# Optimization experiments

Measured on AMD Instinct MI355X. Metric: run time of the kernel, lower is better.

The kernel has to match this reference:

```python
import jax, jax.numpy as jnp
import numpy as np

N_NODES = 50000
N_EDGES = 800000
N_REL = 4
F_IN = 128
H1 = 64          # RGCN out
HEADS = 4
D_H = 32         # per-head GAT out
N_GRAPHS = 64


def setup_inputs() -> dict:
    key = jax.random.key(0)
    ks = jax.random.split(key, 16)
    inp = {
        "x": jax.random.normal(ks[0], (N_NODES, F_IN), dtype=jnp.float32),
        "edge_index": jax.random.randint(ks[1], (2, N_EDGES), 0, N_NODES, dtype=jnp.int32),
        "edge_type": jax.random.randint(ks[2], (N_EDGES,), 0, N_REL, dtype=jnp.int32),
        "batch": jnp.sort(jax.random.randint(ks[3], (N_NODES,), 0, N_GRAPHS, dtype=jnp.int32)),
        # RGCNConv params (relation weights, root weight, bias)
        "W_rel": jax.random.normal(ks[4], (N_REL, F_IN, H1), dtype=jnp.float32) * 0.05,
        "W_root": jax.random.normal(ks[5], (F_IN, H1), dtype=jnp.float32) * 0.05,
        "b_rgcn": jnp.zeros((H1,), dtype=jnp.float32),
        # GATConv params
        "W_gat": jax.random.normal(ks[6], (H1, HEADS * D_H), dtype=jnp.float32) * 0.1,
        "att_src": jax.random.normal(ks[7], (HEADS, D_H), dtype=jnp.float32) * 0.1,
        "att_dst": jax.random.normal(ks[8], (HEADS, D_H), dtype=jnp.float32) * 0.1,
        "b_gat": jnp.zeros((HEADS * D_H,), dtype=jnp.float32),
        # dense layers
        "W1": jax.random.normal(ks[9], (HEADS * D_H, 16), dtype=jnp.float32) * 0.05,
        "b1": jnp.zeros((16,), dtype=jnp.float32),
        "W2": jax.random.normal(ks[10], (16, 1), dtype=jnp.float32) * 0.2,
        "b2": jnp.zeros((1,), dtype=jnp.float32),
    }
    return inp


def reference(x, W_rel, W_root, b_rgcn, W_gat, att_src, att_dst, b_gat,
              W1, b1, W2, b2, edge_index, edge_type, batch):
    src, dst = edge_index[0], edge_index[1]
    n = x.shape[0]

    # ---- RGCNConv: mean aggregation per relation, then linear (linearity lets
    # us aggregate raw features first, then apply W_rel) + root transform ----
    xs = x[src]                                            # [E, F_IN]
    out = x @ W_root + b_rgcn                              # [N, H1]
    for r in range(N_REL):
        mask = (edge_type == r).astype(x.dtype)            # [E]
        s = jax.ops.segment_sum(xs * mask[:, None], dst, num_segments=n)
        cnt = jax.ops.segment_sum(mask, dst, num_segments=n)
        mean_r = s / jnp.maximum(cnt, 1.0)[:, None]        # [N, F_IN]
        out = out + mean_r @ W_rel[r]
    h = jax.nn.relu(out)                                   # [N, H1]
    # (dropout omitted: deterministic/eval reference)

    # ---- GATConv (heads=4, concat, no self loops, edge_attr unused) ----
    g = (h @ W_gat).reshape(n, HEADS, D_H)                 # [N, H, D]
    a_s = jnp.einsum('nhd,hd->nh', g, att_src)             # [N, H]
    a_d = jnp.einsum('nhd,hd->nh', g, att_dst)
    e = jax.nn.leaky_relu(a_s[src] + a_d[dst], 0.2)        # [E, H]
    m = jax.ops.segment_max(e, dst, num_segments=n)        # [N, H]
    ex = jnp.exp(e - m[dst])                               # [E, H]
    den = jax.ops.segment_sum(ex, dst, num_segments=n)     # [N, H]
    alpha = ex / den[dst]
    o = jax.ops.segment_sum(alpha[:, :, None] * g[src], dst, num_segments=n)
    o = o.reshape(n, HEADS * D_H) + b_gat                  # [N, 128]
    o = jax.nn.leaky_relu(o, 0.01)

    # ---- dense1 -> leaky_relu -> global max pool -> dense2 ----
    z = jax.nn.leaky_relu(o @ W1 + b1, 0.01)               # [N, 16]
    p = jax.ops.segment_max(z, batch, num_segments=N_GRAPHS)  # [G, 16]
    y = p @ W2 + b2                                        # [G, 1]
    return y
```

## Files before the change

kernel.cpp:

```cpp
#include <hip/hip_runtime.h>
#include <hip/hip_bf16.h>

constexpr int N_NODES = 50000;
constexpr int N_EDGES = 800000;
constexpr int F_IN = 128;
constexpr int H1 = 64;
constexpr int HEADS = 4;
constexpr int D_H = 32;
constexpr int HOUT = HEADS * D_H;
constexpr int N_REL = 4;
constexpr int N_GRAPHS = 64;
constexpr int MBIG = H1 * (1 + N_REL);
constexpr int NBLK = (N_NODES + 255) / 256;
constexpr int N_PAD = 50048;

typedef __attribute__((ext_vector_type(8))) short bf16x8;
typedef __attribute__((ext_vector_type(4))) float f32x4;

__device__ __forceinline__ unsigned f2mono(float f) {
  unsigned u = __float_as_uint(f);
  return (u & 0x80000000u) ? ~u : (u | 0x80000000u);
}
__device__ __forceinline__ float mono2f(unsigned m) {
  unsigned u = (m & 0x80000000u) ? (m & 0x7FFFFFFFu) : ~m;
  return __uint_as_float(u);
}
constexpr unsigned MONO_NEG_INF = 0x007FFFFFu;

__device__ __forceinline__ unsigned short f2bf(float f) {
  unsigned u = __float_as_uint(f);
  unsigned r = (u + 0x7FFFu + ((u >> 16) & 1u)) >> 16;
  return (unsigned short)r;
}
__device__ __forceinline__ float bf2f(unsigned short h) {
  return __uint_as_float((unsigned)h << 16);
}
__device__ __forceinline__ float bflo(unsigned u) { return __uint_as_float(u << 16); }
__device__ __forceinline__ float bfhi(unsigned u) { return __uint_as_float(u & 0xFFFF0000u); }

constexpr int XCVT_BLOCKS = (N_NODES * (F_IN / 4) + 255) / 256;
constexpr int HIST_BLOCKS = (N_EDGES + 255) / 256;
constexpr int WT_BLOCKS = (MBIG * F_IN + HOUT * H1 + 255) / 256;

__global__ __launch_bounds__(256) void pre_fused(
    const float* __restrict__ x,
    const float* __restrict__ W_root, const float* __restrict__ W_rel,
    const float* __restrict__ W_gat,
    const int* __restrict__ dst,
    unsigned short* __restrict__ xhi, unsigned short* __restrict__ xlo,
    unsigned short* __restrict__ WbT_hi, unsigned short* __restrict__ WbT_lo,
    unsigned short* __restrict__ WgT_hi, unsigned short* __restrict__ WgT_lo,
    int* __restrict__ deg, int* __restrict__ rank,
    unsigned* __restrict__ pm) {
  int b = blockIdx.x;
  if (b < XCVT_BLOCKS) {
    int i = b * 256 + threadIdx.x;
    if (i < N_NODES * (F_IN / 4)) {
      float4 v = reinterpret_cast<const float4*>(x)[i];
      ushort4 hi, lo;
      hi.x = f2bf(v.x); lo.x = f2bf(v.x - bf2f(hi.x));
      hi.y = f2bf(v.y); lo.y = f2bf(v.y - bf2f(hi.y));
      hi.z = f2bf(v.z); lo.z = f2bf(v.z - bf2f(hi.z));
      hi.w = f2bf(v.w); lo.w = f2bf(v.w - bf2f(hi.w));
      reinterpret_cast<ushort4*>(xhi)[i] = hi;
      reinterpret_cast<ushort4*>(xlo)[i] = lo;
    }
  } else if (b < XCVT_BLOCKS + HIST_BLOCKS) {
    int e = (b - XCVT_BLOCKS) * 256 + threadIdx.x;
    if (e < N_EDGES) rank[e] = atomicAdd(&deg[dst[e]], 1);
  } else if (b < XCVT_BLOCKS + HIST_BLOCKS + WT_BLOCKS) {
    int i = (b - XCVT_BLOCKS - HIST_BLOCKS) * 256 + threadIdx.x;
    if (i < MBIG * F_IN) {
      int c = i / F_IN, k = i % F_IN;
      float w = (c < H1) ? W_root[k * H1 + c]
                         : W_rel[((size_t)(((c - H1) >> 6) * F_IN + k)) * H1 + ((c - H1) & 63)];
      unsigned short hi = f2bf(w);
      WbT_hi[i] = hi;
      WbT_lo[i] = f2bf(w - bf2f(hi));
    } else {
      int j = i - MBIG * F_IN;
      if (j < HOUT * H1) {
        int c = j / H1, k = j % H1;
        float w = W_gat[k * HOUT + c];
        unsigned short hi = f2bf(w);
        WgT_hi[j] = hi;
        WgT_lo[j] = f2bf(w - bf2f(hi));
      }
    }
  } else {
    for (int i = threadIdx.x; i < N_GRAPHS * 16; i += 256) pm[i] = MONO_NEG_INF;
  }
}

template <int K>
__device__ __forceinline__ void gemm_body(int bx, int by,
    const unsigned short* __restrict__ Ahi_,
    const unsigned short* __restrict__ Alo_,
    const unsigned short* __restrict__ BT_hi,
    const unsigned short* __restrict__ BT_lo,
    unsigned short* __restrict__ Cbf, int N, int M) {
  __shared__ unsigned short Ah[64 * K];
  __shared__ unsigned short Al[64 * K];
  const int tid = threadIdx.x;
  const int rowBase = bx * 64;
  const int colBase = by * 64;
  constexpr int KQ8 = K / 8;
  for (int s = tid; s < 64 * KQ8; s += 256) {
    int r = s / KQ8, c8 = (s % KQ8) * 8;
    size_t gi = (size_t)(rowBase + r) * K + c8;
    int sw = c8 ^ ((r & 7) << 3);
    *reinterpret_cast<uint4*>(&Ah[r * K + sw]) =
        *reinterpret_cast<const uint4*>(&Ahi_[gi]);
    *reinterpret_cast<uint4*>(&Al[r * K + sw]) =
        *reinterpret_cast<const uint4*>(&Alo_[gi]);
  }
  __syncthreads();
  const int wv = tid >> 6, lane = tid & 63;
  const int wr = (wv >> 1) * 32, wc = (wv & 1) * 32;
  const int lrow = lane & 15, lkc = lane >> 4;
  f32x4 acc[2][2] = {};
#pragma unroll
  for (int ks = 0; ks < K; ks += 32) {
    bf16x8 ah[2], al[2], bh[2], bl[2];
#pragma unroll
    for (int fr = 0; fr < 2; ++fr) {
      int r = wr + fr * 16 + lrow;
      int sw = (ks + lkc * 8) ^ ((r & 7) << 3);
      ah[fr] = *reinterpret_cast<const bf16x8*>(&Ah[r * K + sw]);
      al[fr] = *reinterpret_cast<const bf16x8*>(&Al[r * K + sw]);
    }
#pragma unroll
    for (int fc = 0; fc < 2; ++fc) {
      int c = colBase + wc + fc * 16 + lrow;
      bh[fc] = *reinterpret_cast<const bf16x8*>(&BT_hi[(size_t)c * K + ks + lkc * 8]);
      bl[fc] = *reinterpret_cast<const bf16x8*>(&BT_lo[(size_t)c * K + ks + lkc * 8]);
    }
#pragma unroll
    for (int fr = 0; fr < 2; ++fr)
#pragma unroll
      for (int fc = 0; fc < 2; ++fc) {
        acc[fr][fc] = __builtin_amdgcn_mfma_f32_16x16x32_bf16(ah[fr], bh[fc], acc[fr][fc], 0, 0, 0);
        acc[fr][fc] = __builtin_amdgcn_mfma_f32_16x16x32_bf16(ah[fr], bl[fc], acc[fr][fc], 0, 0, 0);
        acc[fr][fc] = __builtin_amdgcn_mfma_f32_16x16x32_bf16(al[fr], bh[fc], acc[fr][fc], 0, 0, 0);
      }
  }
#pragma unroll
  for (int fr = 0; fr < 2; ++fr) {
#pragma unroll
    for (int i = 0; i < 4; ++i) {
      int row = rowBase + wr + fr * 16 + lkc * 4 + i;
      if (row < N) {
#pragma unroll
        for (int fc = 0; fc < 2; ++fc) {
          int col = colBase + wc + fc * 16 + lrow;
          Cbf[(size_t)row * M + col] = f2bf(acc[fr][fc][i]);
        }
      }
    }
  }
}

constexpr int G1_BX = N_PAD / 64;
constexpr int G1_BLOCKS = G1_BX * (MBIG / 64);
__global__ __launch_bounds__(256) void gemm1_fill(
    const unsigned short* __restrict__ xhi, const unsigned short* __restrict__ xlo,
    const unsigned short* __restrict__ wbt_hi, const unsigned short* __restrict__ wbt_lo,
    unsigned short* __restrict__ xtbf,
    const int* __restrict__ src, const int* __restrict__ dst,
    const int* __restrict__ etype, const int* __restrict__ off,
    const int* __restrict__ rank, int* __restrict__ eprep) {
  if (blockIdx.x < G1_BLOCKS) {
    gemm_body<128>(blockIdx.x % G1_BX, blockIdx.x / G1_BX,
                   xhi, xlo, wbt_hi, wbt_lo, xtbf, N_NODES, MBIG);
  } else {
    int e = (blockIdx.x - G1_BLOCKS) * 256 + threadIdx.x;
    if (e < N_EDGES) {
      int pos = off[dst[e]] + rank[e];
      eprep[pos] = src[e] | (etype[e] << 16);
    }
  }
}

__global__ __launch_bounds__(256) void gemm2_k(
    const unsigned short* __restrict__ hhi, const unsigned short* __restrict__ hlo,
    const unsigned short* __restrict__ wgt_hi, const unsigned short* __restrict__ wgt_lo,
    unsigned short* __restrict__ gbf) {
  gemm_body<64>(blockIdx.x % G1_BX, blockIdx.x / G1_BX,
                hhi, hlo, wgt_hi, wgt_lo, gbf, N_NODES, HOUT);
}

__global__ __launch_bounds__(256) void k_s1(const int* __restrict__ deg,
                                            int* __restrict__ bsum) {
  __shared__ int ss[256];
  int t = threadIdx.x;
  int i = blockIdx.x * 256 + t;
  ss[t] = (i < N_NODES) ? deg[i] : 0;
  __syncthreads();
  for (int d = 128; d > 0; d >>= 1) {
    if (t < d) ss[t] += ss[t + d];
    __syncthreads();
  }
  if (t == 0) bsum[blockIdx.x] = ss[0];
}

__global__ __launch_bounds__(256) void k_s2(const int* __restrict__ bsum,
                                            int* __restrict__ bbase,
                                            int* __restrict__ off) {
  __shared__ int ss[256];
  int t = threadIdx.x;
  int v = (t < NBLK) ? bsum[t] : 0;
  ss[t] = v;
  __syncthreads();
  for (int d = 1; d < 256; d <<= 1) {
    int u = (t >= d) ? ss[t - d] : 0;
    __syncthreads();
    ss[t] += u;
    __syncthreads();
  }
  if (t < NBLK) bbase[t] = ss[t] - v;
  if (t == NBLK - 1) off[N_NODES] = ss[t];
}

__global__ __launch_bounds__(256) void k_s3(const int* __restrict__ deg,
                                            const int* __restrict__ bbase,
                                            int* __restrict__ off) {
  __shared__ int ss[256];
  int t = threadIdx.x;
  int i = blockIdx.x * 256 + t;
  int v = (i < N_NODES) ? deg[i] : 0;
  ss[t] = v;
  __syncthreads();
  for (int d = 1; d < 256; d <<= 1) {
    int u = (t >= d) ? ss[t - d] : 0;
    __syncthreads();
    ss[t] += u;
    __syncthreads();
  }
  if (i < N_NODES) off[i] = bbase[blockIdx.x] + ss[t] - v;
}

__global__ __launch_bounds__(256) void rgcn_gather(const unsigned short* __restrict__ xtbf,
                                                   const int* __restrict__ off,
                                                   const int* __restrict__ eprep,
                                                   const float* __restrict__ b_rgcn,
                                                   unsigned short* __restrict__ hhi,
                                                   unsigned short* __restrict__ hlo) {
  int wid = (blockIdx.x * 256 + threadIdx.x) >> 6;
  int lane = threadIdx.x & 63;
  int half = lane >> 5;
  int cp = lane & 31;
  int start = off[wid], end = off[wid + 1];
  float a0x=0.f,a0y=0.f,a1x=0.f,a1y=0.f,a2x=0.f,a2y=0.f,a3x=0.f,a3y=0.f;
  int c0=0,c1=0,c2=0,c3=0;
  int niter = (end - start + 1) >> 1;
  for (int t = 0; t < niter; t += 2) {
    int idx0 = start + 2 * t + half;
    int idx1 = idx0 + 2;
    int p0 = (idx0 < end) ? eprep[idx0] : 0x70000;
    int p1 = (idx1 < end) ? eprep[idx1] : 0x70000;
    int s0 = p0 & 0xFFFF, r0 = p0 >> 16;
    int s1 = p1 & 0xFFFF, r1 = p1 >> 16;
    unsigned u0 = *reinterpret_cast<const unsigned*>(
        &xtbf[(size_t)s0 * MBIG + H1 + (r0 << 6) + cp * 2]);
    unsigned u1 = *reinterpret_cast<const unsigned*>(
        &xtbf[(size_t)s1 * MBIG + H1 + (r1 << 6) + cp * 2]);
    float v0x = bflo(u0), v0y = bfhi(u0);
    float v1x = bflo(u1), v1y = bfhi(u1);
    a0x += (r0==0)?v0x:0.f; a0y += (r0==0)?v0y:0.f; c0 += (r0==0);
    a1x += (r0==1)?v0x:0.f; a1y += (r0==1)?v0y:0.f; c1 += (r0==1);
    a2x += (r0==2)?v0x:0.f; a2y += (r0==2)?v0y:0.f; c2 += (r0==2);
    a3x += (r0==3)?v0x:0.f; a3y += (r0==3)?v0y:0.f; c3 += (r0==3);
    a0x += (r1==0)?v1x:0.f; a0y += (r1==0)?v1y:0.f; c0 += (r1==0);
    a1x += (r1==1)?v1x:0.f; a1y += (r1==1)?v1y:0.f; c1 += (r1==1);
    a2x += (r1==2)?v1x:0.f; a2y += (r1==2)?v1y:0.f; c2 += (r1==2);
    a3x += (r1==3)?v1x:0.f; a3y += (r1==3)?v1y:0.f; c3 += (r1==3);
  }
  a0x += __shfl_xor(a0x, 32); a0y += __shfl_xor(a0y, 32);
  a1x += __shfl_xor(a1x, 32); a1y += __shfl_xor(a1y, 32);
  a2x += __shfl_xor(a2x, 32); a2y += __shfl_xor(a2y, 32);
  a3x += __shfl_xor(a3x, 32); a3y += __shfl_xor(a3y, 32);
  c0 += __shfl_xor(c0, 32); c1 += __shfl_xor(c1, 32);
  c2 += __shfl_xor(c2, 32); c3 += __shfl_xor(c3, 32);
  if (half == 0) {
    unsigned ur = *reinterpret_cast<const unsigned*>(&xtbf[(size_t)wid * MBIG + cp * 2]);
    float2 bb = *reinterpret_cast<const float2*>(&b_rgcn[cp * 2]);
    float i0 = 1.0f / (float)max(c0, 1);
    float i1 = 1.0f / (float)max(c1, 1);
    float i2 = 1.0f / (float)max(c2, 1);
    float i3 = 1.0f / (float)max(c3, 1);
    float vx = bflo(ur) + bb.x + a0x * i0 + a1x * i1 + a2x * i2 + a3x * i3;
    float vy = bfhi(ur) + bb.y + a0y * i0 + a1y * i1 + a2y * i2 + a3y * i3;
    vx = fmaxf(vx, 0.f);
    vy = fmaxf(vy, 0.f);
    unsigned short hx = f2bf(vx), hy = f2bf(vy);
    ushort2 hv = {hx, hy};
    ushort2 lv = {f2bf(vx - bf2f(hx)), f2bf(vy - bf2f(hy))};
    *reinterpret_cast<ushort2*>(&hhi[(size_t)wid * H1 + cp * 2]) = hv;
    *reinterpret_cast<ushort2*>(&hlo[(size_t)wid * H1 + cp * 2]) = lv;
  }
}

__global__ __launch_bounds__(256) void gat_att(const unsigned short* __restrict__ gbf,
                                               const float* __restrict__ att_src,
                                               const float* __restrict__ att_dst,
                                               float* __restrict__ a_s,
                                               float* __restrict__ a_d) {
  __shared__ float gs[64][129];
  __shared__ float asrc[HOUT], adst[HOUT];
  int t = threadIdx.x;
  if (t < HOUT) { asrc[t] = att_src[t]; adst[t] = att_dst[t]; }
  int nb = blockIdx.x * 64;
#pragma unroll
  for (int it = 0; it < 8; ++it) {
    int idx = it * 256 + t;
    int r = idx >> 5, c4 = (idx & 31) * 4;
    int gn = nb + r;
    uint2 v = make_uint2(0u, 0u);
    if (gn < N_NODES)
      v = *reinterpret_cast<const uint2*>(&gbf[(size_t)gn * HOUT + c4]);
    gs[r][c4 + 0] = bflo(v.x); gs[r][c4 + 1] = bfhi(v.x);
    gs[r][c4 + 2] = bflo(v.y); gs[r][c4 + 3] = bfhi(v.y);
  }
  __syncthreads();
  int n = t & 63, hh = t >> 6;
  float s = 0.f, d = 0.f;
#pragma unroll
  for (int k = 0; k < D_H; ++k) {
    float gv = gs[n][hh * D_H + k];
    s += gv * asrc[hh * D_H + k];
    d += gv * adst[hh * D_H + k];
  }
  if (nb + n < N_NODES) {
    a_s[(size_t)(nb + n) * 4 + hh] = s;
    a_d[(size_t)(nb + n) * 4 + hh] = d;
  }
}

constexpr int GAT_BLOCKS = 2048;
constexpr int GAT_WAVES = GAT_BLOCKS * 4;
__global__ __launch_bounds__(256) void gat_fused(const unsigned short* __restrict__ gbf,
                                                 const float* __restrict__ a_s,
                                                 const float* __restrict__ a_d,
                                                 const int* __restrict__ off,
                                                 const int* __restrict__ eprep,
                                                 const float* __restrict__ b_gat,
                                                 const float* __restrict__ W1,
                                                 const float* __restrict__ b1,
                                                 const int* __restrict__ batch,
                                                 unsigned* __restrict__ p_mono) {
  __shared__ float w1s[HOUT * 16];
  __shared__ float ob[4][HOUT];
  __shared__ unsigned sp[N_GRAPHS * 16];
  const int t = threadIdx.x;
  for (int i = t; i < HOUT * 16; i += 256) w1s[i] = W1[i];
  for (int i = t; i < N_GRAPHS * 16; i += 256) sp[i] = MONO_NEG_INF;
  __syncthreads();
  const int wv = t >> 6, lane = t & 63;
  const int hh = lane >> 4;
  const int jj = lane & 15, grp = lane >> 4;
  const int w = blockIdx.x * 4 + wv;
  const int q = N_NODES / GAT_WAVES;
  const int r = N_NODES % GAT_WAVES;
  const int nbeg = w * q + ((w < r) ? w : r);
  const int ncnt = q + ((w < r) ? 1 : 0);
  for (int wid = nbeg; wid < nbeg + ncnt; ++wid) {
    int start = off[wid], end = off[wid + 1];
    float4 ad4 = *reinterpret_cast<const float4*>(a_d + (size_t)wid * 4);
    float adh = (hh == 0) ? ad4.x : (hh == 1) ? ad4.y : (hh == 2) ? ad4.z : ad4.w;
    float ox = 0.f, oy = 0.f, den = 0.f;
    int i = start;
    for (; i + 4 <= end; i += 4) {
      int p0 = eprep[i], p1 = eprep[i + 1], p2 = eprep[i + 2], p3 = eprep[i + 3];
      int s0 = p0 & 0xFFFF, s1 = p1 & 0xFFFF, s2 = p2 & 0xFFFF, s3 = p3 & 0xFFFF;
      float as0 = a_s[(size_t)s0 * 4 + hh];
      float as1 = a_s[(size_t)s1 * 4 + hh];
      float as2 = a_s[(size_t)s2 * 4 + hh];
      float as3 = a_s[(size_t)s3 * 4 + hh];
      unsigned u0 = *reinterpret_cast<const unsigned*>(&gbf[(size_t)s0 * HOUT + lane * 2]);
      unsigned u1 = *reinterpret_cast<const unsigned*>(&gbf[(size_t)s1 * HOUT + lane * 2]);
      unsigned u2 = *reinterpret_cast<const unsigned*>(&gbf[(size_t)s2 * HOUT + lane * 2]);
      unsigned u3 = *reinterpret_cast<const unsigned*>(&gbf[(size_t)s3 * HOUT + lane * 2]);
      float e0 = as0 + adh; e0 = (e0 > 0.f) ? e0 : 0.2f * e0;
      float e1 = as1 + adh; e1 = (e1 > 0.f) ? e1 : 0.2f * e1;
      float e2 = as2 + adh; e2 = (e2 > 0.f) ? e2 : 0.2f * e2;
      float e3 = as3 + adh; e3 = (e3 > 0.f) ? e3 : 0.2f * e3;
      float x0 = __expf(e0), x1 = __expf(e1), x2 = __expf(e2), x3 = __expf(e3);
      den += x0 + x1 + x2 + x3;
      ox += x0 * bflo(u0) + x1 * bflo(u1) + x2 * bflo(u2) + x3 * bflo(u3);
      oy += x0 * bfhi(u0) + x1 * bfhi(u1) + x2 * bfhi(u2) + x3 * bfhi(u3);
    }
    for (; i < end; ++i) {
      int p = eprep[i];
      int s = p & 0xFFFF;
      float as = a_s[(size_t)s * 4 + hh];
      unsigned u = *reinterpret_cast<const unsigned*>(&gbf[(size_t)s * HOUT + lane * 2]);
      float e = as + adh; e = (e > 0.f) ? e : 0.2f * e;
      float ex = __expf(e);
      den += ex;
      ox += ex * bflo(u);
      oy += ex * bfhi(u);
    }
    float dinv = (den > 0.f) ? (1.0f / den) : 0.f;
    float2 bg = *reinterpret_cast<const float2*>(b_gat + lane * 2);
    float vx = ox * dinv + bg.x; vx = (vx > 0.f) ? vx : 0.01f * vx;
    float vy = oy * dinv + bg.y; vy = (vy > 0.f) ? vy : 0.01f * vy;
    *reinterpret_cast<float2*>(&ob[wv][lane * 2]) = make_float2(vx, vy);
    float acc = 0.f;
#pragma unroll 8
    for (int i2 = 0; i2 < 32; ++i2) {
      int c = grp + 4 * i2;
      acc += ob[wv][c] * w1s[c * 16 + jj];
    }
    acc += __shfl_xor(acc, 16);
    acc += __shfl_xor(acc, 32);
    float z = acc + b1[jj];
    z = (z > 0.f) ? z : 0.01f * z;
    int b = batch[wid];
    if (lane < 16) atomicMax(&sp[b * 16 + jj], f2mono(z));
  }
  __syncthreads();
  for (int i = t; i < N_GRAPHS * 16; i += 256) {
    unsigned v = sp[i];
    if (v != MONO_NEG_INF) atomicMax(p_mono + i, v);
  }
}

__global__ void final_y(const unsigned* __restrict__ p_mono,
                        const float* __restrict__ W2,
                        const float* __restrict__ b2,
                        float* __restrict__ y) {
  int gr = threadIdx.x;
  if (gr >= N_GRAPHS) return;
  float acc = b2[0];
#pragma unroll
  for (int k = 0; k < 16; ++k) acc += mono2f(p_mono[gr * 16 + k]) * W2[k];
  y[gr] = acc;
}

extern "C" void kernel_launch(void* const* d_in, const int* in_sizes, int n_in,
                              void* d_out, int out_size, void* d_ws, size_t ws_size,
                              hipStream_t stream) {
  const float* x       = (const float*)d_in[0];
  const int*   eidx    = (const int*)d_in[1];
  const int*   etype   = (const int*)d_in[2];
  const int*   batch   = (const int*)d_in[3];
  const float* W_rel   = (const float*)d_in[4];
  const float* W_root  = (const float*)d_in[5];
  const float* b_rgcn  = (const float*)d_in[6];
  const float* W_gat   = (const float*)d_in[7];
  const float* att_src = (const float*)d_in[8];
  const float* att_dst = (const float*)d_in[9];
  const float* b_gat   = (const float*)d_in[10];
  const float* W1      = (const float*)d_in[11];
  const float* b1      = (const float*)d_in[12];
  const float* W2      = (const float*)d_in[13];
  const float* b2      = (const float*)d_in[14];
  float* y = (float*)d_out;

  const int* src = eidx;
  const int* dst = eidx + N_EDGES;

  float* ws = (float*)d_ws;
  const size_t OFF_XTBF= 0;
  const size_t OFF_GBF = 0;
  const size_t OFF_XHI = 8007680;
  const size_t OFF_XLO = 11210752;
  const size_t OFF_HHI = 14413824;
  const size_t OFF_HLO = 16015360;
  const size_t OFF_AS  = 17616896;
  const size_t OFF_AD  = 17816896;
  const size_t OFF_PM  = 18016896;
  const size_t OFF_DEG = 18017920;
  const size_t OFF_OFFS= 18067920;
  const size_t OFF_RANK= 18117924;
  const size_t OFF_EP  = 18917924;
  const size_t OFF_BS  = 19717924;
  const size_t OFF_BB  = 19718120;
  const size_t OFF_WBH = 19718320;
  const size_t OFF_WBL = 19738800;
  const size_t OFF_WGH = 19759280;
  const size_t OFF_WGL = 19763376;
  const size_t TOTAL_F = 19767472;
  if (ws_size < TOTAL_F * sizeof(float)) return;

  unsigned short* xtbf = (unsigned short*)(ws + OFF_XTBF);
  unsigned short* gbf  = (unsigned short*)(ws + OFF_GBF);
  unsigned short* xhi  = (unsigned short*)(ws + OFF_XHI);
  unsigned short* xlo  = (unsigned short*)(ws + OFF_XLO);
  unsigned short* hhi  = (unsigned short*)(ws + OFF_HHI);
  unsigned short* hlo  = (unsigned short*)(ws + OFF_HLO);
  float* a_s   = ws + OFF_AS;
  float* a_d   = ws + OFF_AD;
  unsigned* pm = (unsigned*)(ws + OFF_PM);
  int* deg     = (int*)(ws + OFF_DEG);
  int* offs    = (int*)(ws + OFF_OFFS);
  int* rank    = (int*)(ws + OFF_RANK);
  int* eprep   = (int*)(ws + OFF_EP);
  int* bsum    = (int*)(ws + OFF_BS);
  int* bbase   = (int*)(ws + OFF_BB);
  unsigned short* wbt_hi = (unsigned short*)(ws + OFF_WBH);
  unsigned short* wbt_lo = (unsigned short*)(ws + OFF_WBL);
  unsigned short* wgt_hi = (unsigned short*)(ws + OFF_WGH);
  unsigned short* wgt_lo = (unsigned short*)(ws + OFF_WGL);

  hipMemsetAsync(deg, 0, N_NODES * sizeof(int), stream);

  pre_fused<<<XCVT_BLOCKS + HIST_BLOCKS + WT_BLOCKS + 1, 256, 0, stream>>>(
      x, W_root, W_rel, W_gat, dst, xhi, xlo,
      wbt_hi, wbt_lo, wgt_hi, wgt_lo, deg, rank, pm);

  k_s1<<<NBLK, 256, 0, stream>>>(deg, bsum);
  k_s2<<<1, 256, 0, stream>>>(bsum, bbase, offs);
  k_s3<<<NBLK, 256, 0, stream>>>(deg, bbase, offs);

  gemm1_fill<<<G1_BLOCKS + HIST_BLOCKS, 256, 0, stream>>>(
      xhi, xlo, wbt_hi, wbt_lo, xtbf, src, dst, etype, offs, rank, eprep);

  rgcn_gather<<<N_NODES / 4, 256, 0, stream>>>(xtbf, offs, eprep, b_rgcn, hhi, hlo);

  gemm2_k<<<G1_BX * (HOUT / 64), 256, 0, stream>>>(hhi, hlo, wgt_hi, wgt_lo, gbf);

  gat_att<<<(N_NODES + 63) / 64, 256, 0, stream>>>(gbf, att_src, att_dst, a_s, a_d);

  gat_fused<<<GAT_BLOCKS, 256, 0, stream>>>(gbf, a_s, a_d, offs, eprep, b_gat,
                                            W1, b1, batch, pm);

  final_y<<<1, 64, 0, stream>>>(pm, W2, b2, y);
}
```

Baseline: 223.4 us.

## Fold attention vectors into W_gat and compute attention logits in RGCN gather

Precomputes W_gat·att_src and W_gat·att_dst per head (64x4 each) in the prefuse kernel, then computes a_s and a_d directly from the fp32 RGCN output h inside rgcn_gather using a wave shuffle reduction. This removes the separate gat_att kernel launch and its full re-read of the bf16 GAT features. The logits now come from fp32 h rather than bf16-rounded g, which shifts numerics slightly, and the gather kernel takes on extra shuffles.

```diff
diff --git a/kernel.cpp b/kernel.cpp
--- a/kernel.cpp
+++ b/kernel.cpp
@@ -46,12 +46,14 @@
     const float* __restrict__ x,
     const float* __restrict__ W_root, const float* __restrict__ W_rel,
     const float* __restrict__ W_gat,
+    const float* __restrict__ att_src, const float* __restrict__ att_dst,
     const int* __restrict__ dst,
     unsigned short* __restrict__ xhi, unsigned short* __restrict__ xlo,
     unsigned short* __restrict__ WbT_hi, unsigned short* __restrict__ WbT_lo,
     unsigned short* __restrict__ WgT_hi, unsigned short* __restrict__ WgT_lo,
     int* __restrict__ deg, int* __restrict__ rank,
-    unsigned* __restrict__ pm) {
+    unsigned* __restrict__ pm,
+    float* __restrict__ was, float* __restrict__ wad) {
   int b = blockIdx.x;
   if (b < XCVT_BLOCKS) {
     int i = b * 256 + threadIdx.x;
@@ -87,8 +89,20 @@
         WgT_lo[j] = f2bf(w - bf2f(hi));
       }
     }
+  } else if (b == XCVT_BLOCKS + HIST_BLOCKS + WT_BLOCKS) {
+    for (int i = threadIdx.x; i < N_GRAPHS * 16; i += 256) pm[i] = MONO_NEG_INF;
   } else {
-    for (int i = threadIdx.x; i < N_GRAPHS * 16; i += 256) pm[i] = MONO_NEG_INF;
+    int t = threadIdx.x;
+    int k = t >> 2, hh = t & 3;
+    float s = 0.f, d2 = 0.f;
+#pragma unroll 8
+    for (int dd = 0; dd < D_H; ++dd) {
+      float wg = W_gat[k * HOUT + hh * D_H + dd];
+      s += wg * att_src[hh * D_H + dd];
+      d2 += wg * att_dst[hh * D_H + dd];
+    }
+    was[t] = s;
+    wad[t] = d2;
   }
 }
 
@@ -243,8 +257,12 @@
                                                    const int* __restrict__ off,
                                                    const int* __restrict__ eprep,
                                                    const float* __restrict__ b_rgcn,
+                                                   const float* __restrict__ was,
+                                                   const float* __restrict__ wad,
                                                    unsigned short* __restrict__ hhi,
-                                                   unsigned short* __restrict__ hlo) {
+                                                   unsigned short* __restrict__ hlo,
+                                                   float* __restrict__ a_s,
+                                                   float* __restrict__ a_d) {
   int wid = (blockIdx.x * 256 + threadIdx.x) >> 6;
   int lane = threadIdx.x & 63;
   int half = lane >> 5;
@@ -297,42 +315,29 @@
     ushort2 lv = {f2bf(vx - bf2f(hx)), f2bf(vy - bf2f(hy))};
     *reinterpret_cast<ushort2*>(&hhi[(size_t)wid * H1 + cp * 2]) = hv;
     *reinterpret_cast<ushort2*>(&hlo[(size_t)wid * H1 + cp * 2]) = lv;
-  }
-}
-
-__global__ __launch_bounds__(256) void gat_att(const unsigned short* __restrict__ gbf,
-                                               const float* __restrict__ att_src,
-                                               const float* __restrict__ att_dst,
-                                               float* __restrict__ a_s,
-                                               float* __restrict__ a_d) {
-  __shared__ float gs[64][129];
-  __shared__ float asrc[HOUT], adst[HOUT];
-  int t = threadIdx.x;
-  if (t < HOUT) { asrc[t] = att_src[t]; adst[t] = att_dst[t]; }
-  int nb = blockIdx.x * 64;
-#pragma unroll
-  for (int it = 0; it < 8; ++it) {
-    int idx = it * 256 + t;
-    int r = idx >> 5, c4 = (idx & 31) * 4;
-    int gn = nb + r;
-    uint2 v = make_uint2(0u, 0u);
-    if (gn < N_NODES)
-      v = *reinterpret_cast<const uint2*>(&gbf[(size_t)gn * HOUT + c4]);
-    gs[r][c4 + 0] = bflo(v.x); gs[r][c4 + 1] = bfhi(v.x);
-    gs[r][c4 + 2] = bflo(v.y); gs[r][c4 + 3] = bfhi(v.y);
-  }
-  __syncthreads();
-  int n = t & 63, hh = t >> 6;
-  float s = 0.f, d = 0.f;
-#pragma unroll
-  for (int k = 0; k < D_H; ++k) {
-    float gv = gs[n][hh * D_H + k];
-    s += gv * asrc[hh * D_H + k];
-    d += gv * adst[hh * D_H + k];
-  }
-  if (nb + n < N_NODES) {
-    a_s[(size_t)(nb + n) * 4 + hh] = s;
-    a_d[(size_t)(nb + n) * 4 + hh] = d;
+    float4 wsA = *reinterpret_cast<const float4*>(&was[cp * 8]);
+    float4 wsB = *reinterpret_cast<const float4*>(&was[cp * 8 + 4]);
+    float4 wdA = *reinterpret_cast<const float4*>(&wad[cp * 8]);
+    float4 wdB = *reinterpret_cast<const float4*>(&wad[cp * 8 + 4]);
+    float ps0 = vx * wsA.x + vy * wsB.x;
+    float ps1 = vx * wsA.y + vy * wsB.y;
+    float ps2 = vx * wsA.z + vy * wsB.z;
+    float ps3 = vx * wsA.w + vy * wsB.w;
+    float pd0 = vx * wdA.x + vy * wdB.x;
+    float pd1 = vx * wdA.y + vy * wdB.y;
+    float pd2 = vx * wdA.z + vy * wdB.z;
+    float pd3 = vx * wdA.w + vy * wdB.w;
+#pragma unroll
+    for (int d = 1; d < 32; d <<= 1) {
+      ps0 += __shfl_xor(ps0, d); ps1 += __shfl_xor(ps1, d);
+      ps2 += __shfl_xor(ps2, d); ps3 += __shfl_xor(ps3, d);
+      pd0 += __shfl_xor(pd0, d); pd1 += __shfl_xor(pd1, d);
+      pd2 += __shfl_xor(pd2, d); pd3 += __shfl_xor(pd3, d);
+    }
+    if (cp == 0) {
+      *reinterpret_cast<float4*>(&a_s[(size_t)wid * 4]) = make_float4(ps0, ps1, ps2, ps3);
+      *reinterpret_cast<float4*>(&a_d[(size_t)wid * 4]) = make_float4(pd0, pd1, pd2, pd3);
+    }
   }
 }
 
@@ -476,11 +481,13 @@
   const size_t OFF_EP  = 18917924;
   const size_t OFF_BS  = 19717924;
   const size_t OFF_BB  = 19718120;
-  const size_t OFF_WBH = 19718320;
-  const size_t OFF_WBL = 19738800;
-  const size_t OFF_WGH = 19759280;
-  const size_t OFF_WGL = 19763376;
-  const size_t TOTAL_F = 19767472;
+  const size_t OFF_WAS = 19718320;
+  const size_t OFF_WAD = 19718576;
+  const size_t OFF_WBH = 19718832;
+  const size_t OFF_WBL = 19739312;
+  const size_t OFF_WGH = 19759792;
+  const size_t OFF_WGL = 19763888;
+  const size_t TOTAL_F = 19767984;
   if (ws_size < TOTAL_F * sizeof(float)) return;
 
   unsigned short* xtbf = (unsigned short*)(ws + OFF_XTBF);
@@ -498,6 +505,8 @@
   int* eprep   = (int*)(ws + OFF_EP);
   int* bsum    = (int*)(ws + OFF_BS);
   int* bbase   = (int*)(ws + OFF_BB);
+  float* was   = ws + OFF_WAS;
+  float* wad   = ws + OFF_WAD;
   unsigned short* wbt_hi = (unsigned short*)(ws + OFF_WBH);
   unsigned short* wbt_lo = (unsigned short*)(ws + OFF_WBL);
   unsigned short* wgt_hi = (unsigned short*)(ws + OFF_WGH);
@@ -505,9 +514,9 @@
 
   hipMemsetAsync(deg, 0, N_NODES * sizeof(int), stream);
 
-  pre_fused<<<XCVT_BLOCKS + HIST_BLOCKS + WT_BLOCKS + 1, 256, 0, stream>>>(
-      x, W_root, W_rel, W_gat, dst, xhi, xlo,
-      wbt_hi, wbt_lo, wgt_hi, wgt_lo, deg, rank, pm);
+  pre_fused<<<XCVT_BLOCKS + HIST_BLOCKS + WT_BLOCKS + 2, 256, 0, stream>>>(
+      x, W_root, W_rel, W_gat, att_src, att_dst, dst, xhi, xlo,
+      wbt_hi, wbt_lo, wgt_hi, wgt_lo, deg, rank, pm, was, wad);
 
   k_s1<<<NBLK, 256, 0, stream>>>(deg, bsum);
   k_s2<<<1, 256, 0, stream>>>(bsum, bbase, offs);
@@ -516,11 +525,10 @@
   gemm1_fill<<<G1_BLOCKS + HIST_BLOCKS, 256, 0, stream>>>(
       xhi, xlo, wbt_hi, wbt_lo, xtbf, src, dst, etype, offs, rank, eprep);
 
-  rgcn_gather<<<N_NODES / 4, 256, 0, stream>>>(xtbf, offs, eprep, b_rgcn, hhi, hlo);
+  rgcn_gather<<<N_NODES / 4, 256, 0, stream>>>(xtbf, offs, eprep, b_rgcn,
+                                               was, wad, hhi, hlo, a_s, a_d);
 
   gemm2_k<<<G1_BX * (HOUT / 64), 256, 0, stream>>>(hhi, hlo, wgt_hi, wgt_lo, gbf);
-
-  gat_att<<<(N_NODES + 63) / 64, 256, 0, stream>>>(gbf, att_src, att_dst, a_s, a_d);
 
   gat_fused<<<GAT_BLOCKS, 256, 0, stream>>>(gbf, a_s, a_d, offs, eprep, b_gat,
                                             W1, b1, batch, pm);
```

After: 220.3 us. Within noise of the previous version (-1.4%).
